# Kernel tuning notes

Measured on AMD Instinct MI355X. Metric: run time of the kernel, lower is better.

The kernel has to match this reference:

```python
import jax, jax.numpy as jnp
import numpy as np

FORGET_BIAS = 1.0  # TF LSTMCell default


def _lstm_layer(x_tbd, kernel, bias):
    """x_tbd: [T, B, D]; kernel: [D+H, 4H] (gate order i, j, f, o); returns [T, B, H]."""
    H = kernel.shape[1] // 4
    B = x_tbd.shape[1]
    c0 = jnp.zeros((B, H), dtype=x_tbd.dtype)
    h0 = jnp.zeros((B, H), dtype=x_tbd.dtype)

    def step(carry, x_t):
        c, h = carry
        gates = jnp.concatenate([x_t, h], axis=-1) @ kernel + bias
        i, j, f, o = jnp.split(gates, 4, axis=-1)
        c = jax.nn.sigmoid(f + FORGET_BIAS) * c + jax.nn.sigmoid(i) * jnp.tanh(j)
        h = jax.nn.sigmoid(o) * jnp.tanh(c)
        return (c, h), h

    _, hs = jax.lax.scan(step, (c0, h0), x_tbd)
    return hs


def setup_inputs() -> dict:
    key = jax.random.key(0)
    ks = jax.random.split(key, 4)
    B, T, H, C = 64, 1024, 256, 6
    x = jax.random.normal(ks[0], (B, T, H), dtype=jnp.float32)
    kernel0 = jax.random.normal(ks[1], (2 * H, 4 * H), dtype=jnp.float32) * 0.05
    bias0 = jnp.zeros((4 * H,), dtype=jnp.float32)
    kernel1 = jax.random.normal(ks[2], (2 * H, 4 * H), dtype=jnp.float32) * 0.05
    bias1 = jnp.zeros((4 * H,), dtype=jnp.float32)
    w_out = jax.random.normal(ks[3], (H, C), dtype=jnp.float32)
    b_out = jnp.zeros((C,), dtype=jnp.float32)
    return {"x": x, "kernel0": kernel0, "bias0": bias0,
            "kernel1": kernel1, "bias1": bias1,
            "w_out": w_out, "b_out": b_out}


def reference(x, kernel0, bias0, kernel1, bias1, w_out, b_out):
    # testing=True => keep_prob=1.0 (dropout is identity)
    x_tbd = jnp.transpose(x, (1, 0, 2))        # [T, B, D]
    h1 = _lstm_layer(x_tbd, kernel0, bias0)    # [T, B, H]
    h2 = _lstm_layer(h1, kernel1, bias1)       # [T, B, H]
    # sequence_length == T for every batch row => gather last timestep
    last = h2[-1]                              # [B, H]
    logits = last @ w_out + b_out              # [B, C]
    output = jax.nn.sigmoid(logits)
    prediction = jnp.where(output > 0.5,
                           jnp.ones_like(output), jnp.zeros_like(output))
    return logits, output, prediction
```

## Files before the change

kernel.cpp:

```cpp
#include <hip/hip_runtime.h>
#include <math.h>


#define BB 64
#define TT 1024
#define HH 256
#define NTHREADS 512
#define FLAG_BYTES 4096
#define HBUF_FLOATS (BB * HH)
#define WT_FLOATS (256 * 4 * 512)
#define WS_NEEDED (FLAG_BYTES + (size_t)6 * HBUF_FLOATS * 4 + (size_t)2 * WT_FLOATS * 4)
#define HROW 576

typedef float f32x4 __attribute__((ext_vector_type(4)));
typedef int   i32x2 __attribute__((ext_vector_type(2)));

__device__ __forceinline__ void coh_store(float* p, float v) {
  __hip_atomic_store(p, v, __ATOMIC_RELAXED, __HIP_MEMORY_SCOPE_AGENT);
}
__device__ __forceinline__ void coh_store_i(int* p, int v) {
  __hip_atomic_store(p, v, __ATOMIC_RELAXED, __HIP_MEMORY_SCOPE_AGENT);
}

__device__ __forceinline__ void coh_load4(
    const float* p0, const float* p1, const float* p2, const float* p3,
    f32x4& a0, f32x4& a1, f32x4& a2, f32x4& a3) {
  asm volatile(
      "global_load_dwordx4 %0, %4, off sc0 sc1\n\t"
      "global_load_dwordx4 %1, %5, off sc0 sc1\n\t"
      "global_load_dwordx4 %2, %6, off sc0 sc1\n\t"
      "global_load_dwordx4 %3, %7, off sc0 sc1\n\t"
      "s_waitcnt vmcnt(0)"
      : "=&v"(a0), "=&v"(a1), "=&v"(a2), "=&v"(a3)
      : "v"(p0), "v"(p1), "v"(p2), "v"(p3)
      : "memory");
}

__device__ __forceinline__ float fsig(float x) {
  const float e = __builtin_amdgcn_exp2f(x * -1.442695040888963f);
  return __builtin_amdgcn_rcpf(1.0f + e);
}
__device__ __forceinline__ float ftanh(float x) {
  const float e = __builtin_amdgcn_exp2f(x * 2.885390081777927f);
  return 1.0f - 2.0f * __builtin_amdgcn_rcpf(e + 1.0f);
}

__global__ void transpose_w(const float* __restrict__ src, float* __restrict__ dst) {
  __shared__ float t[64][65];
  const int g  = blockIdx.x;
  const int kt = blockIdx.y;
  const int ut = blockIdx.z;
  const int tx = threadIdx.x & 63;
  const int ty = threadIdx.x >> 6;
  #pragma unroll
  for (int r = ty; r < 64; r += 4)
    t[r][tx] = src[(size_t)(kt * 64 + r) * 1024 + g * 256 + ut * 64 + tx];
  __syncthreads();
  #pragma unroll
  for (int r = ty; r < 64; r += 4)
    dst[((size_t)(ut * 64 + r) * 4 + g) * 512 + kt * 64 + tx] = t[tx][r];
}

__global__ __launch_bounds__(NTHREADS, 2) void lstm2_persistent(
    const float* __restrict__ x,
    const float* __restrict__ b0, const float* __restrict__ b1,
    const float* __restrict__ wt0, const float* __restrict__ wt1,
    float* __restrict__ h1buf, float* __restrict__ h2buf,
    int* __restrict__ flags)
{
  __shared__ float hstage[16 * HROW];
  __shared__ f32x4 part[128 * 17];

  const int blk   = blockIdx.x;
  const int taskB = blk >= 128;
  const int tblk  = taskB ? blk - 128 : blk;
  const int bgrp  = tblk >> 5;
  const int ublk  = tblk & 31;

  const int tid  = threadIdx.x;
  const int lane = tid & 63;
  const int wv   = tid >> 6;
  const int ul   = tid & 7;
  const int kq   = (tid >> 3) & 15;
  const int bt   = tid >> 7;
  const bool odd = wv & 1;
  const int r0S  = (wv >> 1) * 4;
  const int cS   = lane + (odd ? 64 : 0);
  const int dposS = cS * 4 + (cS >> 3) * 4;

  const float* WT   = taskB ? wt1 : wt0;
  const float* bias = taskB ? b1 : b0;

  f32x4 w[4][8];
  {
    const float* wb = WT + (size_t)(ublk * 8 + ul) * 2048 + kq * 32;
    #pragma unroll
    for (int g = 0; g < 4; ++g)
      #pragma unroll
      for (int cc = 0; cc < 8; ++cc)
        w[g][cc] = *(const f32x4*)(wb + g * 512 + cc * 4);
  }

  float bi = 0.f, bj = 0.f, bfv = 0.f, bo = 0.f;
  if (tid < 128) {
    const int u = ublk * 8 + (tid & 7);
    bi  = bias[u];
    bj  = bias[256 + u];
    bfv = bias[512 + u];
    bo  = bias[768 + u];
  }
  float cst = 0.f;

  int* myflag = flags + ((size_t)bgrp * 64 + (taskB ? 32 : 0) + ublk) * 2;

  if (!taskB && !odd) {
    const float* bx = x + ((size_t)(bgrp * 16 + r0S) * TT + 0) * HH + lane * 4;
    const size_t rstep = (size_t)TT * HH;
    f32x4 v0 = *(const f32x4*)(bx);
    f32x4 v1 = *(const f32x4*)(bx + rstep);
    f32x4 v2 = *(const f32x4*)(bx + 2 * rstep);
    f32x4 v3 = *(const f32x4*)(bx + 3 * rstep);
    *(f32x4*)&hstage[(r0S + 0) * HROW + dposS] = v0;
    *(f32x4*)&hstage[(r0S + 1) * HROW + dposS] = v1;
    *(f32x4*)&hstage[(r0S + 2) * HROW + dposS] = v2;
    *(f32x4*)&hstage[(r0S + 3) * HROW + dposS] = v3;
  }

  for (int s = 0; s <= TT + 1; ++s) {
    const bool active = taskB ? (s >= 2) : (s < TT);

    if (active) {
      if (odd) {
        const float* src = taskB
            ? (h2buf + (size_t)((s + 1) & 1) * HBUF_FLOATS)
            : (h1buf + (size_t)((s - 1) & 3) * HBUF_FLOATS);
        const float* p0 = src + (size_t)(bgrp * 16 + r0S) * HH + lane * 4;
        f32x4 v0, v1, v2, v3;
        coh_load4(p0, p0 + HH, p0 + 2 * HH, p0 + 3 * HH, v0, v1, v2, v3);
        *(f32x4*)&hstage[(r0S + 0) * HROW + dposS] = v0;
        *(f32x4*)&hstage[(r0S + 1) * HROW + dposS] = v1;
        *(f32x4*)&hstage[(r0S + 2) * HROW + dposS] = v2;
        *(f32x4*)&hstage[(r0S + 3) * HROW + dposS] = v3;
      }

      float acc[4][4];
      #pragma unroll
      for (int b4 = 0; b4 < 4; ++b4)
        #pragma unroll
        for (int g = 0; g < 4; ++g) acc[b4][g] = 0.f;

      const int kbase = kq * 36;
      #pragma unroll
      for (int b4 = 0; b4 < 4; ++b4) {
        const float* hp = &hstage[(bt * 4 + b4) * HROW + kbase];
        #pragma unroll
        for (int cc = 0; cc < 8; ++cc) {
          const f32x4 h4 = *(const f32x4*)(hp + cc * 4);
          #pragma unroll
          for (int g = 0; g < 4; ++g) {
            acc[b4][g] = fmaf(h4[0], w[g][cc][0], acc[b4][g]);
            acc[b4][g] = fmaf(h4[1], w[g][cc][1], acc[b4][g]);
            acc[b4][g] = fmaf(h4[2], w[g][cc][2], acc[b4][g]);
            acc[b4][g] = fmaf(h4[3], w[g][cc][3], acc[b4][g]);
          }
        }
      }

      #pragma unroll
      for (int b4 = 0; b4 < 4; ++b4) {
        f32x4 p = { acc[b4][0], acc[b4][1], acc[b4][2], acc[b4][3] };
        part[((bt * 4 + b4) * 8 + ul) * 17 + kq] = p;
      }
      __syncthreads();

      if (tid < 128) {
        float gi = bi, gj = bj, gf = bfv, go = bo;
        #pragma unroll
        for (int q = 0; q < 16; ++q) {
          const f32x4 p = part[tid * 17 + q];
          gi += p[0]; gj += p[1]; gf += p[2]; go += p[3];
        }
        const float ig = fsig(gi);
        const float jt = ftanh(gj);
        const float fg = fsig(gf + 1.0f);
        const float og = fsig(go);
        cst = fg * cst + ig * jt;
        const float hn = og * ftanh(cst);

        float* hb = taskB
            ? (h2buf + (size_t)(s & 1) * HBUF_FLOATS)
            : (h1buf + (size_t)(s & 3) * HBUF_FLOATS);
        coh_store(hb + (size_t)(bgrp * 16 + (tid >> 3)) * HH + ublk * 8 + (tid & 7), hn);
        asm volatile("s_waitcnt vmcnt(0)" ::: "memory");
      }
    }

    if (s <= TT && tid < 128 && (tid & 63) == 0)
      coh_store_i(myflag + (tid >> 6), s + 1);

    if (!odd) {
      if (!taskB) {
        if (s + 1 < TT) {
          const float* bx = x + ((size_t)(bgrp * 16 + r0S) * TT + (s + 1)) * HH + lane * 4;
          const size_t rstep = (size_t)TT * HH;
          f32x4 v0 = *(const f32x4*)(bx);
          f32x4 v1 = *(const f32x4*)(bx + rstep);
          f32x4 v2 = *(const f32x4*)(bx + 2 * rstep);
          f32x4 v3 = *(const f32x4*)(bx + 3 * rstep);
          *(f32x4*)&hstage[(r0S + 0) * HROW + dposS] = v0;
          *(f32x4*)&hstage[(r0S + 1) * HROW + dposS] = v1;
          *(f32x4*)&hstage[(r0S + 2) * HROW + dposS] = v2;
          *(f32x4*)&hstage[(r0S + 3) * HROW + dposS] = v3;
        }
      } else {
        if (s >= 1 && s <= TT) {
          const float* p0 = h1buf + (size_t)((s - 1) & 3) * HBUF_FLOATS
                          + (size_t)(bgrp * 16 + r0S) * HH + lane * 4;
          f32x4 v0, v1, v2, v3;
          coh_load4(p0, p0 + HH, p0 + 2 * HH, p0 + 3 * HH, v0, v1, v2, v3);
          *(f32x4*)&hstage[(r0S + 0) * HROW + dposS] = v0;
          *(f32x4*)&hstage[(r0S + 1) * HROW + dposS] = v1;
          *(f32x4*)&hstage[(r0S + 2) * HROW + dposS] = v2;
          *(f32x4*)&hstage[(r0S + 3) * HROW + dposS] = v3;
        }
      }
    }

    if (s <= TT) {
      if (tid < 64) {
        const int* fp = flags + ((size_t)bgrp * 64 + tid) * 2;
        for (;;) {
          i32x2 f;
          asm volatile(
              "global_load_dwordx2 %0, %1, off sc0 sc1\n\t"
              "s_waitcnt vmcnt(0)"
              : "=v"(f) : "v"(fp) : "memory");
          const int v = f[0] < f[1] ? f[0] : f[1];
          if (__all(v >= s + 1)) break;
        }
      }
      __syncthreads();
    }
  }
}

__global__ void head_kernel(const float* __restrict__ h2last,
                            const float* __restrict__ w_out,
                            const float* __restrict__ b_out,
                            float* __restrict__ out)
{
  int tid = threadIdx.x;
  if (tid >= 384) return;
  int bb = tid / 6, cc = tid % 6;
  float acc = b_out[cc];
  const float* hr = h2last + bb * HH;
  #pragma unroll 4
  for (int uu = 0; uu < HH; ++uu) acc = fmaf(hr[uu], w_out[uu * 6 + cc], acc);
  out[tid] = acc;
  float sg = 1.f / (1.f + expf(-acc));
  out[384 + tid] = sg;
  out[768 + tid] = (sg > 0.5f) ? 1.f : 0.f;
}

extern "C" void kernel_launch(void* const* d_in, const int* in_sizes, int n_in,
                              void* d_out, int out_size, void* d_ws, size_t ws_size,
                              hipStream_t stream) {
  const float* x     = (const float*)d_in[0];
  const float* k0    = (const float*)d_in[1];
  const float* b0    = (const float*)d_in[2];
  const float* k1    = (const float*)d_in[3];
  const float* b1    = (const float*)d_in[4];
  const float* w_out = (const float*)d_in[5];
  const float* b_out = (const float*)d_in[6];
  float* out = (float*)d_out;

  if (ws_size < WS_NEEDED) return;

  int*   flags = (int*)d_ws;
  float* h1b   = (float*)((char*)d_ws + FLAG_BYTES);
  float* h2b   = h1b + 4 * HBUF_FLOATS;
  float* wt0   = h2b + 2 * HBUF_FLOATS;
  float* wt1   = wt0 + WT_FLOATS;

  hipMemsetAsync(d_ws, 0, FLAG_BYTES + (size_t)6 * HBUF_FLOATS * 4, stream);

  transpose_w<<<dim3(4, 8, 4), 256, 0, stream>>>(k0, wt0);
  transpose_w<<<dim3(4, 8, 4), 256, 0, stream>>>(k1, wt1);

  lstm2_persistent<<<256, NTHREADS, 0, stream>>>(x, b0, b1, wt0, wt1,
                                                 h1b, h2b, flags);

  head_kernel<<<1, 384, 0, stream>>>(h2b + HBUF_FLOATS, w_out, b_out, out);
}
```

Before: 3.991 ms.

## Replace global barrier flags with value-tagged data polling and deep ring buffers

Drops the per-step all-block flag barrier. Each stored h value now carries a step-dependent offset, and consumers spin on the data itself until every value falls inside the expected tag window, then subtract the tag. The h buffers become a 16-deep ring so layer 1 can run ahead of layer 2. A sparse flag from layer 2 provides back-pressure, and the partial-sum scratch is double-buffered to avoid a second barrier per step. In exchange the tag encoding costs some float precision, since adding up to 128 to h loses low mantissa bits, and correctness depends on the tag windows never aliasing.

```diff
diff --git a/kernel.cpp b/kernel.cpp
--- a/kernel.cpp
+++ b/kernel.cpp
@@ -6,22 +6,36 @@
 #define TT 1024
 #define HH 256
 #define NTHREADS 512
+#define DEPTH 16
 #define FLAG_BYTES 4096
 #define HBUF_FLOATS (BB * HH)
 #define WT_FLOATS (256 * 4 * 512)
-#define WS_NEEDED (FLAG_BYTES + (size_t)6 * HBUF_FLOATS * 4 + (size_t)2 * WT_FLOATS * 4)
+#define WS_NEEDED (FLAG_BYTES + (size_t)2 * DEPTH * HBUF_FLOATS * 4 + (size_t)2 * WT_FLOATS * 4)
 #define HROW 576
 
 typedef float f32x4 __attribute__((ext_vector_type(4)));
-typedef int   i32x2 __attribute__((ext_vector_type(2)));
-
+
+__device__ __forceinline__ float emap(int s) {
+  return (float)(((s & 31) + 1) * 4);
+}
 __device__ __forceinline__ void coh_store(float* p, float v) {
   __hip_atomic_store(p, v, __ATOMIC_RELAXED, __HIP_MEMORY_SCOPE_AGENT);
 }
 __device__ __forceinline__ void coh_store_i(int* p, int v) {
   __hip_atomic_store(p, v, __ATOMIC_RELAXED, __HIP_MEMORY_SCOPE_AGENT);
 }
-
+__device__ __forceinline__ int ld_flag(const int* p) {
+  int v;
+  asm volatile("global_load_dword %0, %1, off sc0 sc1\n\ts_waitcnt vmcnt(0)"
+               : "=v"(v) : "v"(p) : "memory");
+  return v;
+}
+__device__ __forceinline__ float ld_scout(const float* p) {
+  float v;
+  asm volatile("global_load_dword %0, %1, off sc0 sc1\n\ts_waitcnt vmcnt(0)"
+               : "=v"(v) : "v"(p) : "memory");
+  return v;
+}
 __device__ __forceinline__ void coh_load4(
     const float* p0, const float* p1, const float* p2, const float* p3,
     f32x4& a0, f32x4& a1, f32x4& a2, f32x4& a3) {
@@ -34,6 +48,27 @@
       : "=&v"(a0), "=&v"(a1), "=&v"(a2), "=&v"(a3)
       : "v"(p0), "v"(p1), "v"(p2), "v"(p3)
       : "memory");
+}
+__device__ __forceinline__ bool ok4(f32x4 v, float e) {
+  const float m0 = fmaxf(fabsf(v[0] - e), fabsf(v[1] - e));
+  const float m1 = fmaxf(fabsf(v[2] - e), fabsf(v[3] - e));
+  return fmaxf(m0, m1) <= 1.0f;
+}
+__device__ __forceinline__ void gather_poll(
+    const float* p0, int rs, float e,
+    f32x4& a0, f32x4& a1, f32x4& a2, f32x4& a3) {
+  for (;;) {
+    const float v = ld_scout(p0);
+    if (__all(fabsf(v - e) <= 1.0f)) break;
+    __builtin_amdgcn_s_sleep(2);
+  }
+  for (;;) {
+    coh_load4(p0, p0 + rs, p0 + 2 * rs, p0 + 3 * rs, a0, a1, a2, a3);
+    const bool ok = ok4(a0, e) && ok4(a1, e) && ok4(a2, e) && ok4(a3, e);
+    if (__all(ok)) break;
+    __builtin_amdgcn_s_sleep(2);
+  }
+  a0 -= e; a1 -= e; a2 -= e; a3 -= e;
 }
 
 __device__ __forceinline__ float fsig(float x) {
@@ -61,15 +96,23 @@
     dst[((size_t)(ut * 64 + r) * 4 + g) * 512 + kt * 64 + tx] = t[tx][r];
 }
 
+__global__ void init_sentinels(float* __restrict__ h1b, float* __restrict__ h2b) {
+  const int i = blockIdx.x * blockDim.x + threadIdx.x;
+  if (i < HBUF_FLOATS) {
+    h1b[(size_t)15 * HBUF_FLOATS + i] = 128.0f;
+    h2b[(size_t)15 * HBUF_FLOATS + i] = 128.0f;
+  }
+}
+
 __global__ __launch_bounds__(NTHREADS, 2) void lstm2_persistent(
     const float* __restrict__ x,
     const float* __restrict__ b0, const float* __restrict__ b1,
     const float* __restrict__ wt0, const float* __restrict__ wt1,
     float* __restrict__ h1buf, float* __restrict__ h2buf,
-    int* __restrict__ flags)
+    int* __restrict__ l2f)
 {
   __shared__ float hstage[16 * HROW];
-  __shared__ f32x4 part[128 * 17];
+  __shared__ f32x4 part[2][128 * 17];
 
   const int blk   = blockIdx.x;
   const int taskB = blk >= 128;
@@ -84,7 +127,7 @@
   const int kq   = (tid >> 3) & 15;
   const int bt   = tid >> 7;
   const bool odd = wv & 1;
-  const int r0S  = (wv >> 1) * 4;
+  const int r0S  = bt * 4;
   const int cS   = lane + (odd ? 64 : 0);
   const int dposS = cS * 4 + (cS >> 3) * 4;
 
@@ -111,135 +154,95 @@
   }
   float cst = 0.f;
 
-  int* myflag = flags + ((size_t)bgrp * 64 + (taskB ? 32 : 0) + ublk) * 2;
-
-  if (!taskB && !odd) {
-    const float* bx = x + ((size_t)(bgrp * 16 + r0S) * TT + 0) * HH + lane * 4;
-    const size_t rstep = (size_t)TT * HH;
-    f32x4 v0 = *(const f32x4*)(bx);
-    f32x4 v1 = *(const f32x4*)(bx + rstep);
-    f32x4 v2 = *(const f32x4*)(bx + 2 * rstep);
-    f32x4 v3 = *(const f32x4*)(bx + 3 * rstep);
+  const size_t browoff = (size_t)(bgrp * 16 + r0S) * HH + lane * 4;
+
+  for (int s = 0; s < TT; ++s) {
+    const float ecur  = emap(s);
+    const float eprev = emap(s - 1);
+    const int   scur  = s & 15;
+    const int   sprev = (s + 15) & 15;
+
+    f32x4 v0, v1, v2, v3;
+    if (!odd) {
+      if (!taskB) {
+        const float* bx = x + ((size_t)(bgrp * 16 + r0S) * TT + s) * HH + lane * 4;
+        const size_t rstep = (size_t)TT * HH;
+        v0 = *(const f32x4*)(bx);
+        v1 = *(const f32x4*)(bx + rstep);
+        v2 = *(const f32x4*)(bx + 2 * rstep);
+        v3 = *(const f32x4*)(bx + 3 * rstep);
+      } else {
+        const float* p0 = h1buf + (size_t)scur * HBUF_FLOATS + browoff;
+        gather_poll(p0, HH, ecur, v0, v1, v2, v3);
+      }
+    } else {
+      const float* p0 = (taskB ? h2buf : h1buf) + (size_t)sprev * HBUF_FLOATS + browoff;
+      gather_poll(p0, HH, eprev, v0, v1, v2, v3);
+    }
     *(f32x4*)&hstage[(r0S + 0) * HROW + dposS] = v0;
     *(f32x4*)&hstage[(r0S + 1) * HROW + dposS] = v1;
     *(f32x4*)&hstage[(r0S + 2) * HROW + dposS] = v2;
     *(f32x4*)&hstage[(r0S + 3) * HROW + dposS] = v3;
-  }
-
-  for (int s = 0; s <= TT + 1; ++s) {
-    const bool active = taskB ? (s >= 2) : (s < TT);
-
-    if (active) {
-      if (odd) {
-        const float* src = taskB
-            ? (h2buf + (size_t)((s + 1) & 1) * HBUF_FLOATS)
-            : (h1buf + (size_t)((s - 1) & 3) * HBUF_FLOATS);
-        const float* p0 = src + (size_t)(bgrp * 16 + r0S) * HH + lane * 4;
-        f32x4 v0, v1, v2, v3;
-        coh_load4(p0, p0 + HH, p0 + 2 * HH, p0 + 3 * HH, v0, v1, v2, v3);
-        *(f32x4*)&hstage[(r0S + 0) * HROW + dposS] = v0;
-        *(f32x4*)&hstage[(r0S + 1) * HROW + dposS] = v1;
-        *(f32x4*)&hstage[(r0S + 2) * HROW + dposS] = v2;
-        *(f32x4*)&hstage[(r0S + 3) * HROW + dposS] = v3;
-      }
-
-      float acc[4][4];
+
+    float acc[4][4];
+    #pragma unroll
+    for (int b4 = 0; b4 < 4; ++b4)
       #pragma unroll
-      for (int b4 = 0; b4 < 4; ++b4)
+      for (int g = 0; g < 4; ++g) acc[b4][g] = 0.f;
+
+    const int kbase = kq * 36;
+    #pragma unroll
+    for (int b4 = 0; b4 < 4; ++b4) {
+      const float* hp = &hstage[(r0S + b4) * HROW + kbase];
+      #pragma unroll
+      for (int cc = 0; cc < 8; ++cc) {
+        const f32x4 h4 = *(const f32x4*)(hp + cc * 4);
         #pragma unroll
-        for (int g = 0; g < 4; ++g) acc[b4][g] = 0.f;
-
-      const int kbase = kq * 36;
-      #pragma unroll
-      for (int b4 = 0; b4 < 4; ++b4) {
-        const float* hp = &hstage[(bt * 4 + b4) * HROW + kbase];
-        #pragma unroll
-        for (int cc = 0; cc < 8; ++cc) {
-          const f32x4 h4 = *(const f32x4*)(hp + cc * 4);
-          #pragma unroll
-          for (int g = 0; g < 4; ++g) {
-            acc[b4][g] = fmaf(h4[0], w[g][cc][0], acc[b4][g]);
-            acc[b4][g] = fmaf(h4[1], w[g][cc][1], acc[b4][g]);
-            acc[b4][g] = fmaf(h4[2], w[g][cc][2], acc[b4][g]);
-            acc[b4][g] = fmaf(h4[3], w[g][cc][3], acc[b4][g]);
-          }
-        }
-      }
-
-      #pragma unroll
-      for (int b4 = 0; b4 < 4; ++b4) {
-        f32x4 p = { acc[b4][0], acc[b4][1], acc[b4][2], acc[b4][3] };
-        part[((bt * 4 + b4) * 8 + ul) * 17 + kq] = p;
-      }
-      __syncthreads();
-
-      if (tid < 128) {
-        float gi = bi, gj = bj, gf = bfv, go = bo;
-        #pragma unroll
-        for (int q = 0; q < 16; ++q) {
-          const f32x4 p = part[tid * 17 + q];
-          gi += p[0]; gj += p[1]; gf += p[2]; go += p[3];
-        }
-        const float ig = fsig(gi);
-        const float jt = ftanh(gj);
-        const float fg = fsig(gf + 1.0f);
-        const float og = fsig(go);
-        cst = fg * cst + ig * jt;
-        const float hn = og * ftanh(cst);
-
-        float* hb = taskB
-            ? (h2buf + (size_t)(s & 1) * HBUF_FLOATS)
-            : (h1buf + (size_t)(s & 3) * HBUF_FLOATS);
-        coh_store(hb + (size_t)(bgrp * 16 + (tid >> 3)) * HH + ublk * 8 + (tid & 7), hn);
-        asm volatile("s_waitcnt vmcnt(0)" ::: "memory");
-      }
-    }
-
-    if (s <= TT && tid < 128 && (tid & 63) == 0)
-      coh_store_i(myflag + (tid >> 6), s + 1);
-
-    if (!odd) {
-      if (!taskB) {
-        if (s + 1 < TT) {
-          const float* bx = x + ((size_t)(bgrp * 16 + r0S) * TT + (s + 1)) * HH + lane * 4;
-          const size_t rstep = (size_t)TT * HH;
-          f32x4 v0 = *(const f32x4*)(bx);
-          f32x4 v1 = *(const f32x4*)(bx + rstep);
-          f32x4 v2 = *(const f32x4*)(bx + 2 * rstep);
-          f32x4 v3 = *(const f32x4*)(bx + 3 * rstep);
-          *(f32x4*)&hstage[(r0S + 0) * HROW + dposS] = v0;
-          *(f32x4*)&hstage[(r0S + 1) * HROW + dposS] = v1;
-          *(f32x4*)&hstage[(r0S + 2) * HROW + dposS] = v2;
-          *(f32x4*)&hstage[(r0S + 3) * HROW + dposS] = v3;
-        }
-      } else {
-        if (s >= 1 && s <= TT) {
-          const float* p0 = h1buf + (size_t)((s - 1) & 3) * HBUF_FLOATS
-                          + (size_t)(bgrp * 16 + r0S) * HH + lane * 4;
-          f32x4 v0, v1, v2, v3;
-          coh_load4(p0, p0 + HH, p0 + 2 * HH, p0 + 3 * HH, v0, v1, v2, v3);
-          *(f32x4*)&hstage[(r0S + 0) * HROW + dposS] = v0;
-          *(f32x4*)&hstage[(r0S + 1) * HROW + dposS] = v1;
-          *(f32x4*)&hstage[(r0S + 2) * HROW + dposS] = v2;
-          *(f32x4*)&hstage[(r0S + 3) * HROW + dposS] = v3;
+        for (int g = 0; g < 4; ++g) {
+          acc[b4][g] = fmaf(h4[0], w[g][cc][0], acc[b4][g]);
+          acc[b4][g] = fmaf(h4[1], w[g][cc][1], acc[b4][g]);
+          acc[b4][g] = fmaf(h4[2], w[g][cc][2], acc[b4][g]);
+          acc[b4][g] = fmaf(h4[3], w[g][cc][3], acc[b4][g]);
         }
       }
     }
 
-    if (s <= TT) {
-      if (tid < 64) {
-        const int* fp = flags + ((size_t)bgrp * 64 + tid) * 2;
+    #pragma unroll
+    for (int b4 = 0; b4 < 4; ++b4) {
+      f32x4 p = { acc[b4][0], acc[b4][1], acc[b4][2], acc[b4][3] };
+      part[s & 1][((r0S + b4) * 8 + ul) * 17 + kq] = p;
+    }
+    __syncthreads();
+
+    if (tid < 128) {
+      float gi = bi, gj = bj, gf = bfv, go = bo;
+      #pragma unroll
+      for (int q = 0; q < 16; ++q) {
+        const f32x4 p = part[s & 1][tid * 17 + q];
+        gi += p[0]; gj += p[1]; gf += p[2]; go += p[3];
+      }
+      const float ig = fsig(gi);
+      const float jt = ftanh(gj);
+      const float fg = fsig(gf + 1.0f);
+      const float og = fsig(go);
+      cst = fg * cst + ig * jt;
+      const float hn = og * ftanh(cst);
+
+      if (!taskB && s >= DEPTH) {
+        const int thr = s - (DEPTH - 1);
+        const int* fp = l2f + bgrp * 32 + (lane & 31);
         for (;;) {
-          i32x2 f;
-          asm volatile(
-              "global_load_dwordx2 %0, %1, off sc0 sc1\n\t"
-              "s_waitcnt vmcnt(0)"
-              : "=v"(f) : "v"(fp) : "memory");
-          const int v = f[0] < f[1] ? f[0] : f[1];
-          if (__all(v >= s + 1)) break;
+          const int f = (lane < 32) ? ld_flag(fp) : thr;
+          if (__all(f >= thr)) break;
+          __builtin_amdgcn_s_sleep(2);
         }
       }
-      __syncthreads();
+
+      float* hb = (taskB ? h2buf : h1buf) + (size_t)scur * HBUF_FLOATS;
+      coh_store(hb + (size_t)(bgrp * 16 + (tid >> 3)) * HH + ublk * 8 + (tid & 7),
+                hn + ecur);
+
+      if (taskB && tid == 0) coh_store_i(l2f + bgrp * 32 + ublk, s + 1);
     }
   }
 }
@@ -255,7 +258,8 @@
   float acc = b_out[cc];
   const float* hr = h2last + bb * HH;
   #pragma unroll 4
-  for (int uu = 0; uu < HH; ++uu) acc = fmaf(hr[uu], w_out[uu * 6 + cc], acc);
+  for (int uu = 0; uu < HH; ++uu)
+    acc = fmaf(hr[uu] - 128.0f, w_out[uu * 6 + cc], acc);
   out[tid] = acc;
   float sg = 1.f / (1.f + expf(-acc));
   out[384 + tid] = sg;
@@ -276,19 +280,22 @@
 
   if (ws_size < WS_NEEDED) return;
 
-  int*   flags = (int*)d_ws;
-  float* h1b   = (float*)((char*)d_ws + FLAG_BYTES);
-  float* h2b   = h1b + 4 * HBUF_FLOATS;
-  float* wt0   = h2b + 2 * HBUF_FLOATS;
-  float* wt1   = wt0 + WT_FLOATS;
-
-  hipMemsetAsync(d_ws, 0, FLAG_BYTES + (size_t)6 * HBUF_FLOATS * 4, stream);
+  int*   l2f = (int*)d_ws;
+  float* h1b = (float*)((char*)d_ws + FLAG_BYTES);
+  float* h2b = h1b + (size_t)DEPTH * HBUF_FLOATS;
+  float* wt0 = h2b + (size_t)DEPTH * HBUF_FLOATS;
+  float* wt1 = wt0 + WT_FLOATS;
+
+  hipMemsetAsync(d_ws, 0,
+                 FLAG_BYTES + (size_t)2 * DEPTH * HBUF_FLOATS * 4, stream);
+  init_sentinels<<<64, 256, 0, stream>>>(h1b, h2b);
 
   transpose_w<<<dim3(4, 8, 4), 256, 0, stream>>>(k0, wt0);
   transpose_w<<<dim3(4, 8, 4), 256, 0, stream>>>(k1, wt1);
 
   lstm2_persistent<<<256, NTHREADS, 0, stream>>>(x, b0, b1, wt0, wt1,
-                                                 h1b, h2b, flags);
-
-  head_kernel<<<1, 384, 0, stream>>>(h2b + HBUF_FLOATS, w_out, b_out, out);
-}
+                                                 h1b, h2b, l2f);
+
+  head_kernel<<<1, 384, 0, stream>>>(h2b + (size_t)15 * HBUF_FLOATS,
+                                     w_out, b_out, out);
+}
```

New measurement: 5.242 ms. 1.31x slower.
